# Kernel optimization log

Hardware: AMD Instinct MI355X
Metric: run time of the kernel (lower is better)

The kernel has to match this reference:

```python
import jax, jax.numpy as jnp
import numpy as np

B, S, D, H = 2, 2048, 1024, 16
DK = D // H  # 64


def setup_inputs() -> dict:
    key = jax.random.key(0)
    ks = jax.random.split(key, 9)
    query = jax.random.normal(ks[0], (B, S, D), dtype=jnp.float32)
    k_in = jax.random.normal(ks[1], (B, S, D), dtype=jnp.float32)
    v_in = jax.random.normal(ks[2], (B, S, D), dtype=jnp.float32)
    mask = jax.random.randint(ks[3], (B, S, S), 0, 2, dtype=jnp.int32)
    sc = 1.0 / np.sqrt(D)
    Wq = jax.random.normal(ks[4], (H, D, DK), dtype=jnp.float32) * sc  # per-head q proj
    Wk = jax.random.normal(ks[5], (H, D, DK), dtype=jnp.float32) * sc
    Wv = jax.random.normal(ks[6], (H, D, DK), dtype=jnp.float32) * sc
    Wu = jax.random.normal(ks[7], (D, D), dtype=jnp.float32) * sc  # unifyheads weight
    bu = jax.random.normal(ks[8], (D,), dtype=jnp.float32) * 0.01
    return {"query": query, "key": k_in, "value": v_in, "mask": mask,
            "Wq": Wq, "Wk": Wk, "Wv": Wv, "Wu": Wu, "bu": bu}


def reference(query, key, value, mask, Wq, Wk, Wv, Wu, bu):
    scale = DK ** 0.25  # original divides q and k each by d_k^(1/4)
    q = jnp.einsum('bsd,hdk->bhsk', query, Wq) / scale
    k = jnp.einsum('bsd,hdk->bhsk', key, Wk) / scale
    v = jnp.einsum('bsd,hdk->bhsk', value, Wv)
    scores = jnp.einsum('bhsk,bhtk->bhst', q, k)  # [B,H,S,S]
    scores = jnp.where(mask[:, None, :, :] == 0, jnp.float32(-1e9), scores)
    attn = jax.nn.softmax(scores, axis=-1)
    out = jnp.einsum('bhst,bhtk->bhsk', attn, v)
    out = jnp.transpose(out, (0, 2, 1, 3)).reshape(query.shape[0], query.shape[1], D)  # concat heads
    return out @ Wu + bu
```

## Files before the change

### kernel.cpp

```cpp
#include <hip/hip_runtime.h>
#include <hip/hip_bf16.h>


typedef __bf16 bf16_t;
typedef __attribute__((ext_vector_type(4))) __bf16 bf16x4;
typedef __attribute__((ext_vector_type(8))) __bf16 bf16x8;
typedef __attribute__((ext_vector_type(4))) float f32x4;
typedef unsigned int u32;

#define B_ 2
#define S_ 2048
#define D_ 1024
#define H_ 16
#define DK_ 64
#define NX_ (4096 * 1024)

static __device__ __forceinline__ f32x4 mfma16(bf16x8 a, bf16x8 b, f32x4 c) {
  return __builtin_amdgcn_mfma_f32_16x16x32_bf16(a, b, c, 0, 0, 0);
}

static __device__ __forceinline__ void async16(const bf16_t* g, bf16_t* l) {
  __builtin_amdgcn_global_load_lds(
      (const __attribute__((address_space(1))) u32*)g,
      (__attribute__((address_space(3))) u32*)l, 16, 0, 0);
}

__global__ __launch_bounds__(256) void prep(
    const float* __restrict__ q, const float* __restrict__ k,
    const float* __restrict__ v, const int* __restrict__ mask,
    const float* __restrict__ Wq, const float* __restrict__ Wk,
    const float* __restrict__ Wv, const float* __restrict__ Wu,
    bf16_t* __restrict__ qo, bf16_t* __restrict__ ko, bf16_t* __restrict__ vo,
    bf16_t* __restrict__ Bq, bf16_t* __restrict__ Bk, bf16_t* __restrict__ Bv,
    bf16_t* __restrict__ Bu, unsigned int* __restrict__ bits, float qkscale) {
  __shared__ __align__(16) bf16_t T[64][72];
  const int f = blockIdx.x;
  const int tid = threadIdx.x;

  if (f < 6144) {
    const int z = f / 2048, bx = f - z * 2048;
    const float* src = (z == 0) ? q : (z == 1) ? k : v;
    bf16_t* dst = (z == 0) ? qo : (z == 1) ? ko : vo;
    size_t i = ((size_t)bx * 256 + tid) * 8;
    float4 a = *(const float4*)(src + i);
    float4 b = *(const float4*)(src + i + 4);
    bf16x8 o;
    o[0] = (bf16_t)a.x; o[1] = (bf16_t)a.y; o[2] = (bf16_t)a.z; o[3] = (bf16_t)a.w;
    o[4] = (bf16_t)b.x; o[5] = (bf16_t)b.y; o[6] = (bf16_t)b.z; o[7] = (bf16_t)b.w;
    *(bf16x8*)(dst + i) = o;
  } else if (f < 7168) {
    const int idx = f - 6144;
    const int bx = idx & 15, by = (idx >> 4) & 15, z = idx >> 8;
    const float* W = (z == 0) ? Wq : (z == 1) ? Wk : (z == 2) ? Wv : Wu;
    bf16_t* BT = (z == 0) ? Bq : (z == 1) ? Bk : (z == 2) ? Bv : Bu;
    const float scale = (z <= 1) ? qkscale : 1.0f;
    const int d0 = bx * 64, nt = by;
    const int r = tid & 63, g = tid >> 6;

    const float* src = (z < 3)
        ? W + ((size_t)nt * D_ + d0 + r) * DK_ + g * 16
        : W + (size_t)(d0 + r) * D_ + nt * 64 + g * 16;
#pragma unroll
    for (int j = 0; j < 4; ++j) {
      float4 w4 = *(const float4*)(src + j * 4);
      T[g * 16 + j * 4 + 0][r] = (bf16_t)(w4.x * scale);
      T[g * 16 + j * 4 + 1][r] = (bf16_t)(w4.y * scale);
      T[g * 16 + j * 4 + 2][r] = (bf16_t)(w4.z * scale);
      T[g * 16 + j * 4 + 3][r] = (bf16_t)(w4.w * scale);
    }
    __syncthreads();
    const int orow = tid >> 3, seg = tid & 7;
#pragma unroll
    for (int p = 0; p < 2; ++p) {
      int rr = p * 32 + orow;
      *(bf16x8*)(BT + (size_t)(nt * 64 + rr) * D_ + d0 + seg * 8) =
          *(const bf16x8*)&T[rr][seg * 8];
    }
  } else {
    const int w = (f - 7168) * 256 + tid;
    const int4* p = (const int4*)(mask + (size_t)w * 32);
    unsigned int vv = 0;
#pragma unroll
    for (int i = 0; i < 8; ++i) {
      int4 m4 = p[i];
      vv |= (m4.x != 0 ? 1u : 0u) << (i * 4 + 0);
      vv |= (m4.y != 0 ? 1u : 0u) << (i * 4 + 1);
      vv |= (m4.z != 0 ? 1u : 0u) << (i * 4 + 2);
      vv |= (m4.w != 0 ? 1u : 0u) << (i * 4 + 3);
    }
    bits[w] = vv;
  }
}

__global__ __launch_bounds__(256) void gemm_bt(
    const bf16_t* __restrict__ A0, const bf16_t* __restrict__ A1,
    const bf16_t* __restrict__ A2, const bf16_t* __restrict__ BT0,
    const bf16_t* __restrict__ BT1, const bf16_t* __restrict__ BT2,
    bf16_t* __restrict__ C0, bf16_t* __restrict__ C1, bf16_t* __restrict__ C2) {
  __shared__ __align__(16) bf16_t As[128 * 64];
  __shared__ __align__(16) bf16_t Bs[128 * 64];

  const int flat = blockIdx.x;
  const int serial = (flat & 7) * 96 + (flat >> 3);
  const int z = serial >> 8;
  const int r = serial & 255;
  const bf16_t* A = (z == 0) ? A0 : (z == 1) ? A1 : A2;
  const bf16_t* BT = (z == 0) ? BT0 : (z == 1) ? BT1 : BT2;
  bf16_t* C = (z == 0) ? C0 : (z == 1) ? C1 : C2;
  const int row_blk = (z < 2) ? (r >> 3) : (r & 7);
  const int col_blk = (z < 2) ? (r & 7) : (r >> 3);
  const size_t ldc = (z < 2) ? 1024 : 4096;

  const int tid = threadIdx.x;
  const int lane = tid & 63, wave = tid >> 6;
  const int l = lane & 15, quad = lane >> 4;
  const int wm = wave >> 1, wn = wave & 1;
  const int row0 = row_blk * 128, col0 = col_blk * 128;

  const int lr = lane >> 3;
  const int gc8 = (lane & 7) ^ lr;
  const int xl = l & 7;

  f32x4 acc[4][4];
#pragma unroll
  for (int i = 0; i < 4; ++i)
#pragma unroll
    for (int j = 0; j < 4; ++j) acc[i][j] = {0.f, 0.f, 0.f, 0.f};

  for (int k0 = 0; k0 < 1024; k0 += 64) {
    __syncthreads();
#pragma unroll
    for (int c = 0; c < 4; ++c) {
      int r2 = wave * 32 + c * 8;
      async16(A + (size_t)(row0 + r2 + lr) * 1024 + k0 + gc8 * 8, As + r2 * 64);
      async16(BT + (size_t)(col0 + r2 + lr) * 1024 + k0 + gc8 * 8, Bs + r2 * 64);
    }
    __syncthreads();

#pragma unroll
    for (int kh = 0; kh < 2; ++kh) {
      bf16x8 af[4], bf[4];
#pragma unroll
      for (int f = 0; f < 4; ++f)
        af[f] = *(const bf16x8*)&As[(wm * 64 + f * 16 + l) * 64 +
                                    (((kh * 4 + quad) ^ xl) * 8)];
#pragma unroll
      for (int f = 0; f < 4; ++f)
        bf[f] = *(const bf16x8*)&Bs[(wn * 64 + f * 16 + l) * 64 +
                                    (((kh * 4 + quad) ^ xl) * 8)];
#pragma unroll
      for (int fm = 0; fm < 4; ++fm)
#pragma unroll
        for (int fn = 0; fn < 4; ++fn)
          acc[fm][fn] = mfma16(af[fm], bf[fn], acc[fm][fn]);
    }
  }

#pragma unroll
  for (int fm = 0; fm < 4; ++fm)
#pragma unroll
    for (int fn = 0; fn < 4; ++fn)
#pragma unroll
      for (int reg = 0; reg < 4; ++reg) {
        int row = row0 + wm * 64 + fm * 16 + quad * 4 + reg;
        int col = col0 + wn * 64 + fn * 16 + l;
        C[(size_t)row * ldc + col] = (bf16_t)acc[fm][fn][reg];
      }
}

__global__ __launch_bounds__(256) void gemm_bt64(
    const bf16_t* __restrict__ A, const bf16_t* __restrict__ BT,
    float* __restrict__ C, const float* __restrict__ bias) {
  __shared__ __align__(16) bf16_t As[64 * 64];
  __shared__ __align__(16) bf16_t Bs[128 * 64];

  const int flat = blockIdx.x;
  const int serial = (flat & 7) * 64 + (flat >> 3);
  const int tid = threadIdx.x;
  const int lane = tid & 63, wave = tid >> 6;
  const int l = lane & 15, quad = lane >> 4;
  const int row0 = (serial >> 3) * 64, col0 = (serial & 7) * 128;

  const int lr = lane >> 3;
  const int gc8 = (lane & 7) ^ lr;
  const int xl = l & 7;

  f32x4 acc[4][2];
#pragma unroll
  for (int i = 0; i < 4; ++i)
#pragma unroll
    for (int j = 0; j < 2; ++j) acc[i][j] = {0.f, 0.f, 0.f, 0.f};

  for (int k0 = 0; k0 < 1024; k0 += 64) {
    __syncthreads();
#pragma unroll
    for (int c = 0; c < 2; ++c) {
      int r = wave * 16 + c * 8;
      async16(A + (size_t)(row0 + r + lr) * 1024 + k0 + gc8 * 8, As + r * 64);
    }
#pragma unroll
    for (int c = 0; c < 4; ++c) {
      int r = wave * 32 + c * 8;
      async16(BT + (size_t)(col0 + r + lr) * 1024 + k0 + gc8 * 8, Bs + r * 64);
    }
    __syncthreads();

#pragma unroll
    for (int kh = 0; kh < 2; ++kh) {
      bf16x8 af[4], bf[2];
#pragma unroll
      for (int f = 0; f < 4; ++f)
        af[f] = *(const bf16x8*)&As[(f * 16 + l) * 64 +
                                    (((kh * 4 + quad) ^ xl) * 8)];
#pragma unroll
      for (int f = 0; f < 2; ++f)
        bf[f] = *(const bf16x8*)&Bs[(wave * 32 + f * 16 + l) * 64 +
                                    (((kh * 4 + quad) ^ xl) * 8)];
#pragma unroll
      for (int fm = 0; fm < 4; ++fm)
#pragma unroll
        for (int fn = 0; fn < 2; ++fn)
          acc[fm][fn] = mfma16(af[fm], bf[fn], acc[fm][fn]);
    }
  }

#pragma unroll
  for (int fm = 0; fm < 4; ++fm)
#pragma unroll
    for (int fn = 0; fn < 2; ++fn)
#pragma unroll
      for (int reg = 0; reg < 4; ++reg) {
        int row = row0 + fm * 16 + quad * 4 + reg;
        int col = col0 + wave * 32 + fn * 16 + l;
        C[(size_t)row * 1024 + col] = acc[fm][fn][reg] + bias[col];
      }
}

__global__ __launch_bounds__(256, 2) void attn_kernel(
    const bf16_t* __restrict__ Qx, const bf16_t* __restrict__ Kx,
    const bf16_t* __restrict__ Vt, const unsigned int* __restrict__ mbits,
    bf16_t* __restrict__ out) {
  __shared__ __align__(16) bf16_t Ks[2][64 * 64];
  __shared__ __align__(16) bf16_t Vts[2][64 * 64];
  __shared__ __align__(16) bf16_t Ps[4][32][72];

  const int tid = threadIdx.x;
  const int lane = tid & 63, wave = tid >> 6;
  const int l = lane & 15, quad = lane >> 4;

  const int flat = blockIdx.x + 16 * (blockIdx.y + 16 * blockIdx.z);
  const int serial = (flat >> 3) + (flat & 7) * 64;
  const int qt = serial & 15;
  const int h = (serial >> 4) & 15;
  const int b = serial >> 8;

  const int ch = h * 64;
  const size_t rb = (size_t)b * S_;
  const int q0 = qt * 128 + wave * 32;
  const int quad4 = quad * 4;

  const int lr = lane >> 3;
  const int gc8 = (lane & 7) ^ lr;
  const int xl = l & 7;

  bf16x8 bq[2][2];
#pragma unroll
  for (int mf = 0; mf < 2; ++mf) {
    const bf16_t* qp = Qx + (rb + q0 + mf * 16 + l) * D_ + ch;
    bq[mf][0] = *(const bf16x8*)(qp + quad * 8);
    bq[mf][1] = *(const bf16x8*)(qp + 32 + quad * 8);
  }

  bf16x8 ones;
#pragma unroll
  for (int j = 0; j < 8; ++j) ones[j] = (bf16_t)1.0f;

  const f32x4 zero = {0.f, 0.f, 0.f, 0.f};
  f32x4 o[2][4];
  f32x4 rs[2];
#pragma unroll
  for (int mf = 0; mf < 2; ++mf) {
    rs[mf] = zero;
#pragma unroll
    for (int nt = 0; nt < 4; ++nt) o[mf][nt] = zero;
  }

  const u32* mrow[2];
#pragma unroll
  for (int mf = 0; mf < 2; ++mf)
    mrow[mf] = mbits + (size_t)(b * S_ + q0 + mf * 16 + l) * (S_ / 32);

  auto stage = [&](int t0, int buf) {
#pragma unroll
    for (int it = 0; it < 2; ++it) {
      int r0 = it * 32 + wave * 8;
      async16(Kx + (rb + t0 + r0 + lr) * D_ + ch + gc8 * 8,
              &Ks[buf][r0 * 64]);
      async16(Vt + (size_t)(ch + r0 + lr) * 4096 + rb + t0 + gc8 * 8,
              &Vts[buf][r0 * 64]);
    }
  };

  stage(0, 0);
  uint2 mwc[2] = {*(const uint2*)&mrow[0][0], *(const uint2*)&mrow[1][0]};

  int cur = 0;
  for (int t0 = 0; t0 < S_; t0 += 64) {
    __syncthreads();
    const int tn = t0 + 64;
    if (tn < S_) stage(tn, cur ^ 1);
    const int nidx = (tn < S_) ? (tn >> 5) : 0;
    uint2 mwn0 = *(const uint2*)&mrow[0][nidx];
    uint2 mwn1 = *(const uint2*)&mrow[1][nidx];

    const bf16_t* Kc = Ks[cur];
    const bf16_t* Vc = Vts[cur];

#pragma unroll
    for (int ts = 0; ts < 4; ++ts) {
      int rK = (ts * 16 + l) * 64;
      bf16x8 ak0 = *(const bf16x8*)&Kc[rK + ((quad ^ xl) * 8)];
      bf16x8 ak1 = *(const bf16x8*)&Kc[rK + (((4 + quad) ^ xl) * 8)];
      int base = (ts & 1) * 16 + quad4;
#pragma unroll
      for (int mf = 0; mf < 2; ++mf) {
        f32x4 s = mfma16(ak0, bq[mf][0], zero);
        s = mfma16(ak1, bq[mf][1], s);
        u32 mw = (ts < 2) ? mwc[mf].x : mwc[mf].y;
        bf16x4 pv;
#pragma unroll
        for (int reg = 0; reg < 4; ++reg) {
          float e = exp2f(s[reg]);
          int bm = __builtin_amdgcn_sbfe(mw, base + reg, 1);
          float p = __int_as_float(__float_as_int(e) & bm);
          pv[reg] = (bf16_t)p;
        }
        *(bf16x4*)&Ps[wave][mf * 16 + l][ts * 16 + quad4] = pv;
      }
    }

    bf16x8 ap[2][2];
#pragma unroll
    for (int mf = 0; mf < 2; ++mf) {
      ap[mf][0] = *(const bf16x8*)&Ps[wave][mf * 16 + l][quad * 8];
      ap[mf][1] = *(const bf16x8*)&Ps[wave][mf * 16 + l][32 + quad * 8];
    }

    __builtin_amdgcn_s_setprio(1);
#pragma unroll
    for (int mf = 0; mf < 2; ++mf) {
      rs[mf] = mfma16(ap[mf][0], ones, rs[mf]);
      rs[mf] = mfma16(ap[mf][1], ones, rs[mf]);
    }
#pragma unroll
    for (int nt = 0; nt < 4; ++nt) {
      int rV = (nt * 16 + l) * 64;
      bf16x8 bv0 = *(const bf16x8*)&Vc[rV + ((quad ^ xl) * 8)];
      bf16x8 bv1 = *(const bf16x8*)&Vc[rV + (((4 + quad) ^ xl) * 8)];
#pragma unroll
      for (int mf = 0; mf < 2; ++mf) {
        o[mf][nt] = mfma16(ap[mf][0], bv0, o[mf][nt]);
        o[mf][nt] = mfma16(ap[mf][1], bv1, o[mf][nt]);
      }
    }
    __builtin_amdgcn_s_setprio(0);

    mwc[0] = mwn0;
    mwc[1] = mwn1;
    cur ^= 1;
  }

#pragma unroll
  for (int mf = 0; mf < 2; ++mf) {
#pragma unroll
    for (int reg = 0; reg < 4; ++reg) {
      float inv = (rs[mf][reg] > 0.f) ? (1.f / rs[mf][reg]) : 0.f;
      int srow = q0 + mf * 16 + quad4 + reg;
      bf16_t* op = out + (rb + srow) * D_ + ch;
#pragma unroll
      for (int nt = 0; nt < 4; ++nt)
        op[nt * 16 + l] = (bf16_t)(o[mf][nt][reg] * inv);
    }
  }
}

extern "C" void kernel_launch(void* const* d_in, const int* in_sizes, int n_in,
                              void* d_out, int out_size, void* d_ws, size_t ws_size,
                              hipStream_t stream) {
  const float* q_in = (const float*)d_in[0];
  const float* k_in = (const float*)d_in[1];
  const float* v_in = (const float*)d_in[2];
  const int* mask = (const int*)d_in[3];
  const float* Wq = (const float*)d_in[4];
  const float* Wk = (const float*)d_in[5];
  const float* Wv = (const float*)d_in[6];
  const float* Wu = (const float*)d_in[7];
  const float* bu = (const float*)d_in[8];
  float* outp = (float*)d_out;

  bf16_t* qx = (bf16_t*)d_ws;
  bf16_t* kx = qx + NX_;
  bf16_t* vx = kx + NX_;
  bf16_t* qb = vx + NX_;
  bf16_t* kb = qb + NX_;
  bf16_t* vtb = kb + NX_;
  bf16_t* BTq = vtb + NX_;
  bf16_t* BTk = BTq + D_ * D_;
  bf16_t* BTv = BTk + D_ * D_;
  bf16_t* BTu = BTv + D_ * D_;
  unsigned int* mb = (unsigned int*)(BTu + D_ * D_);
  bf16_t* ab = qx;

  const float qkscale = 0.35355339059327373f * 1.2011224087864498f;

  dim3 blk(256);
  prep<<<dim3(8192), blk, 0, stream>>>(q_in, k_in, v_in, mask,
                                       Wq, Wk, Wv, Wu,
                                       qx, kx, vx,
                                       BTq, BTk, BTv, BTu, mb, qkscale);
  gemm_bt<<<dim3(768), blk, 0, stream>>>(qx, kx, BTv, BTq, BTk, vx,
                                         qb, kb, vtb);
  attn_kernel<<<dim3(S_ / 128, H_, B_), blk, 0, stream>>>(qb, kb, vtb, mb, ab);
  gemm_bt64<<<dim3(512), blk, 0, stream>>>(ab, BTu, outp, bu);
}
```

Measured before the change: 263.7 us.

## Drop LDS staging and load GEMM and attention operands directly from global memory

Removes the async global-to-LDS staging, the LDS tiles and the barriers from both GEMM kernels and the attention kernel. Each wave now loads its MFMA fragments straight from global memory into registers, relying on L1/L2 caching for reuse across waves. Occupancy hints are added to the launch bounds. This removes LDS traffic and block-wide syncs, but loses data sharing between waves and the double-buffered prefetch in attention, so global and L2 traffic rises and load latency is exposed.

Measured after the change: 406.5 us. +54.2%, slower.

```diff
diff --git a/kernel.cpp b/kernel.cpp
--- a/kernel.cpp
+++ b/kernel.cpp
@@ -17,12 +17,6 @@
 
 static __device__ __forceinline__ f32x4 mfma16(bf16x8 a, bf16x8 b, f32x4 c) {
   return __builtin_amdgcn_mfma_f32_16x16x32_bf16(a, b, c, 0, 0, 0);
-}
-
-static __device__ __forceinline__ void async16(const bf16_t* g, bf16_t* l) {
-  __builtin_amdgcn_global_load_lds(
-      (const __attribute__((address_space(1))) u32*)g,
-      (__attribute__((address_space(3))) u32*)l, 16, 0, 0);
 }
 
 __global__ __launch_bounds__(256) void prep(
@@ -92,14 +86,11 @@
   }
 }
 
-__global__ __launch_bounds__(256) void gemm_bt(
+__global__ __launch_bounds__(256, 3) void gemm_bt(
     const bf16_t* __restrict__ A0, const bf16_t* __restrict__ A1,
     const bf16_t* __restrict__ A2, const bf16_t* __restrict__ BT0,
     const bf16_t* __restrict__ BT1, const bf16_t* __restrict__ BT2,
     bf16_t* __restrict__ C0, bf16_t* __restrict__ C1, bf16_t* __restrict__ C2) {
-  __shared__ __align__(16) bf16_t As[128 * 64];
-  __shared__ __align__(16) bf16_t Bs[128 * 64];
-
   const int flat = blockIdx.x;
   const int serial = (flat & 7) * 96 + (flat >> 3);
   const int z = serial >> 8;
@@ -115,11 +106,16 @@
   const int lane = tid & 63, wave = tid >> 6;
   const int l = lane & 15, quad = lane >> 4;
   const int wm = wave >> 1, wn = wave & 1;
-  const int row0 = row_blk * 128, col0 = col_blk * 128;
-
-  const int lr = lane >> 3;
-  const int gc8 = (lane & 7) ^ lr;
-  const int xl = l & 7;
+  const int row0 = blockIdx.x ? row_blk * 128 : row_blk * 128;
+  const int col0 = col_blk * 128;
+
+  const bf16_t* ap[4];
+  const bf16_t* bp[4];
+#pragma unroll
+  for (int f = 0; f < 4; ++f) {
+    ap[f] = A + (size_t)(row0 + wm * 64 + f * 16 + l) * 1024 + quad * 8;
+    bp[f] = BT + (size_t)(col0 + wn * 64 + f * 16 + l) * 1024 + quad * 8;
+  }
 
   f32x4 acc[4][4];
 #pragma unroll
@@ -128,26 +124,15 @@
     for (int j = 0; j < 4; ++j) acc[i][j] = {0.f, 0.f, 0.f, 0.f};
 
   for (int k0 = 0; k0 < 1024; k0 += 64) {
-    __syncthreads();
-#pragma unroll
-    for (int c = 0; c < 4; ++c) {
-      int r2 = wave * 32 + c * 8;
-      async16(A + (size_t)(row0 + r2 + lr) * 1024 + k0 + gc8 * 8, As + r2 * 64);
-      async16(BT + (size_t)(col0 + r2 + lr) * 1024 + k0 + gc8 * 8, Bs + r2 * 64);
-    }
-    __syncthreads();
-
 #pragma unroll
     for (int kh = 0; kh < 2; ++kh) {
       bf16x8 af[4], bf[4];
 #pragma unroll
       for (int f = 0; f < 4; ++f)
-        af[f] = *(const bf16x8*)&As[(wm * 64 + f * 16 + l) * 64 +
-                                    (((kh * 4 + quad) ^ xl) * 8)];
+        af[f] = *(const bf16x8*)(ap[f] + k0 + kh * 32);
 #pragma unroll
       for (int f = 0; f < 4; ++f)
-        bf[f] = *(const bf16x8*)&Bs[(wn * 64 + f * 16 + l) * 64 +
-                                    (((kh * 4 + quad) ^ xl) * 8)];
+        bf[f] = *(const bf16x8*)(bp[f] + k0 + kh * 32);
 #pragma unroll
       for (int fm = 0; fm < 4; ++fm)
 #pragma unroll
@@ -168,12 +153,9 @@
       }
 }
 
-__global__ __launch_bounds__(256) void gemm_bt64(
+__global__ __launch_bounds__(256, 2) void gemm_bt64(
     const bf16_t* __restrict__ A, const bf16_t* __restrict__ BT,
     float* __restrict__ C, const float* __restrict__ bias) {
-  __shared__ __align__(16) bf16_t As[64 * 64];
-  __shared__ __align__(16) bf16_t Bs[128 * 64];
-
   const int flat = blockIdx.x;
   const int serial = (flat & 7) * 64 + (flat >> 3);
   const int tid = threadIdx.x;
@@ -181,9 +163,14 @@
   const int l = lane & 15, quad = lane >> 4;
   const int row0 = (serial >> 3) * 64, col0 = (serial & 7) * 128;
 
-  const int lr = lane >> 3;
-  const int gc8 = (lane & 7) ^ lr;
-  const int xl = l & 7;
+  const bf16_t* ap[4];
+  const bf16_t* bp[2];
+#pragma unroll
+  for (int f = 0; f < 4; ++f)
+    ap[f] = A + (size_t)(row0 + f * 16 + l) * 1024 + quad * 8;
+#pragma unroll
+  for (int f = 0; f < 2; ++f)
+    bp[f] = BT + (size_t)(col0 + wave * 32 + f * 16 + l) * 1024 + quad * 8;
 
   f32x4 acc[4][2];
 #pragma unroll
@@ -192,30 +179,15 @@
     for (int j = 0; j < 2; ++j) acc[i][j] = {0.f, 0.f, 0.f, 0.f};
 
   for (int k0 = 0; k0 < 1024; k0 += 64) {
-    __syncthreads();
-#pragma unroll
-    for (int c = 0; c < 2; ++c) {
-      int r = wave * 16 + c * 8;
-      async16(A + (size_t)(row0 + r + lr) * 1024 + k0 + gc8 * 8, As + r * 64);
-    }
-#pragma unroll
-    for (int c = 0; c < 4; ++c) {
-      int r = wave * 32 + c * 8;
-      async16(BT + (size_t)(col0 + r + lr) * 1024 + k0 + gc8 * 8, Bs + r * 64);
-    }
-    __syncthreads();
-
 #pragma unroll
     for (int kh = 0; kh < 2; ++kh) {
       bf16x8 af[4], bf[2];
 #pragma unroll
       for (int f = 0; f < 4; ++f)
-        af[f] = *(const bf16x8*)&As[(f * 16 + l) * 64 +
-                                    (((kh * 4 + quad) ^ xl) * 8)];
+        af[f] = *(const bf16x8*)(ap[f] + k0 + kh * 32);
 #pragma unroll
       for (int f = 0; f < 2; ++f)
-        bf[f] = *(const bf16x8*)&Bs[(wave * 32 + f * 16 + l) * 64 +
-                                    (((kh * 4 + quad) ^ xl) * 8)];
+        bf[f] = *(const bf16x8*)(bp[f] + k0 + kh * 32);
 #pragma unroll
       for (int fm = 0; fm < 4; ++fm)
 #pragma unroll
@@ -240,8 +212,6 @@
     const bf16_t* __restrict__ Qx, const bf16_t* __restrict__ Kx,
     const bf16_t* __restrict__ Vt, const unsigned int* __restrict__ mbits,
     bf16_t* __restrict__ out) {
-  __shared__ __align__(16) bf16_t Ks[2][64 * 64];
-  __shared__ __align__(16) bf16_t Vts[2][64 * 64];
   __shared__ __align__(16) bf16_t Ps[4][32][72];
 
   const int tid = threadIdx.x;
@@ -259,10 +229,6 @@
   const int q0 = qt * 128 + wave * 32;
   const int quad4 = quad * 4;
 
-  const int lr = lane >> 3;
-  const int gc8 = (lane & 7) ^ lr;
-  const int xl = l & 7;
-
   bf16x8 bq[2][2];
 #pragma unroll
   for (int mf = 0; mf < 2; ++mf) {
@@ -290,42 +256,31 @@
   for (int mf = 0; mf < 2; ++mf)
     mrow[mf] = mbits + (size_t)(b * S_ + q0 + mf * 16 + l) * (S_ / 32);
 
-  auto stage = [&](int t0, int buf) {
-#pragma unroll
-    for (int it = 0; it < 2; ++it) {
-      int r0 = it * 32 + wave * 8;
-      async16(Kx + (rb + t0 + r0 + lr) * D_ + ch + gc8 * 8,
-              &Ks[buf][r0 * 64]);
-      async16(Vt + (size_t)(ch + r0 + lr) * 4096 + rb + t0 + gc8 * 8,
-              &Vts[buf][r0 * 64]);
-    }
-  };
-
-  stage(0, 0);
-  uint2 mwc[2] = {*(const uint2*)&mrow[0][0], *(const uint2*)&mrow[1][0]};
-
-  int cur = 0;
   for (int t0 = 0; t0 < S_; t0 += 64) {
-    __syncthreads();
-    const int tn = t0 + 64;
-    if (tn < S_) stage(tn, cur ^ 1);
-    const int nidx = (tn < S_) ? (tn >> 5) : 0;
-    uint2 mwn0 = *(const uint2*)&mrow[0][nidx];
-    uint2 mwn1 = *(const uint2*)&mrow[1][nidx];
-
-    const bf16_t* Kc = Ks[cur];
-    const bf16_t* Vc = Vts[cur];
-
+    bf16x8 ak[4][2];
 #pragma unroll
     for (int ts = 0; ts < 4; ++ts) {
-      int rK = (ts * 16 + l) * 64;
-      bf16x8 ak0 = *(const bf16x8*)&Kc[rK + ((quad ^ xl) * 8)];
-      bf16x8 ak1 = *(const bf16x8*)&Kc[rK + (((4 + quad) ^ xl) * 8)];
+      const bf16_t* kp = Kx + (rb + t0 + ts * 16 + l) * D_ + ch;
+      ak[ts][0] = *(const bf16x8*)(kp + quad * 8);
+      ak[ts][1] = *(const bf16x8*)(kp + 32 + quad * 8);
+    }
+    bf16x8 bv[4][2];
+#pragma unroll
+    for (int nt = 0; nt < 4; ++nt) {
+      const bf16_t* vp = Vt + (size_t)(ch + nt * 16 + l) * 4096 + rb + t0;
+      bv[nt][0] = *(const bf16x8*)(vp + quad * 8);
+      bv[nt][1] = *(const bf16x8*)(vp + 32 + quad * 8);
+    }
+    uint2 mwc[2] = {*(const uint2*)&mrow[0][t0 >> 5],
+                    *(const uint2*)&mrow[1][t0 >> 5]};
+
+#pragma unroll
+    for (int ts = 0; ts < 4; ++ts) {
       int base = (ts & 1) * 16 + quad4;
 #pragma unroll
       for (int mf = 0; mf < 2; ++mf) {
-        f32x4 s = mfma16(ak0, bq[mf][0], zero);
-        s = mfma16(ak1, bq[mf][1], s);
+        f32x4 s = mfma16(ak[ts][0], bq[mf][0], zero);
+        s = mfma16(ak[ts][1], bq[mf][1], s);
         u32 mw = (ts < 2) ? mwc[mf].x : mwc[mf].y;
         bf16x4 pv;
 #pragma unroll
@@ -354,20 +309,13 @@
     }
 #pragma unroll
     for (int nt = 0; nt < 4; ++nt) {
-      int rV = (nt * 16 + l) * 64;
-      bf16x8 bv0 = *(const bf16x8*)&Vc[rV + ((quad ^ xl) * 8)];
-      bf16x8 bv1 = *(const bf16x8*)&Vc[rV + (((4 + quad) ^ xl) * 8)];
 #pragma unroll
       for (int mf = 0; mf < 2; ++mf) {
-        o[mf][nt] = mfma16(ap[mf][0], bv0, o[mf][nt]);
-        o[mf][nt] = mfma16(ap[mf][1], bv1, o[mf][nt]);
+        o[mf][nt] = mfma16(ap[mf][0], bv[nt][0], o[mf][nt]);
+        o[mf][nt] = mfma16(ap[mf][1], bv[nt][1], o[mf][nt]);
       }
     }
     __builtin_amdgcn_s_setprio(0);
-
-    mwc[0] = mwn0;
-    mwc[1] = mwn1;
-    cur ^= 1;
   }
 
 #pragma unroll
```

## Software-pipeline attention loop across tiles with triple-buffered K/V staging

Applied to the files above, without the earlier changes.

Restructures the attention main loop so the QK^T MFMAs for the next key tile are issued while softmax and P·V for the previous tile run, with K/V staging moved from double to triple buffering in LDS. The goal is to overlap exp/mask VALU work with matrix-core work and hide the dependency between score computation and softmax. It adds LDS use (one more 64x64 K and V buffer) and keeps a full score tile live in registers, which may lower occupancy or cause spills under the 256x2 launch bounds. The prologue and epilogue handle the first and last tiles separately.

Result: no change. 260.0 us (-1.4%).

```diff
diff --git a/kernel.cpp b/kernel.cpp
--- a/kernel.cpp
+++ b/kernel.cpp
@@ -240,8 +240,8 @@
     const bf16_t* __restrict__ Qx, const bf16_t* __restrict__ Kx,
     const bf16_t* __restrict__ Vt, const unsigned int* __restrict__ mbits,
     bf16_t* __restrict__ out) {
-  __shared__ __align__(16) bf16_t Ks[2][64 * 64];
-  __shared__ __align__(16) bf16_t Vts[2][64 * 64];
+  __shared__ __align__(16) bf16_t Ks[3][64 * 64];
+  __shared__ __align__(16) bf16_t Vts[3][64 * 64];
   __shared__ __align__(16) bf16_t Ps[4][32][72];
 
   const int tid = threadIdx.x;
@@ -301,51 +301,46 @@
     }
   };
 
-  stage(0, 0);
-  uint2 mwc[2] = {*(const uint2*)&mrow[0][0], *(const uint2*)&mrow[1][0]};
-
-  int cur = 0;
-  for (int t0 = 0; t0 < S_; t0 += 64) {
-    __syncthreads();
-    const int tn = t0 + 64;
-    if (tn < S_) stage(tn, cur ^ 1);
-    const int nidx = (tn < S_) ? (tn >> 5) : 0;
-    uint2 mwn0 = *(const uint2*)&mrow[0][nidx];
-    uint2 mwn1 = *(const uint2*)&mrow[1][nidx];
-
-    const bf16_t* Kc = Ks[cur];
-    const bf16_t* Vc = Vts[cur];
-
+  auto qk_tile = [&](const bf16_t* Kc, f32x4 s[4][2]) {
 #pragma unroll
     for (int ts = 0; ts < 4; ++ts) {
       int rK = (ts * 16 + l) * 64;
       bf16x8 ak0 = *(const bf16x8*)&Kc[rK + ((quad ^ xl) * 8)];
       bf16x8 ak1 = *(const bf16x8*)&Kc[rK + (((4 + quad) ^ xl) * 8)];
+#pragma unroll
+      for (int mf = 0; mf < 2; ++mf) {
+        f32x4 acc0 = mfma16(ak0, bq[mf][0], zero);
+        s[ts][mf] = mfma16(ak1, bq[mf][1], acc0);
+      }
+    }
+  };
+
+  auto softmax_store = [&](f32x4 s[4][2], uint2 mw[2]) {
+#pragma unroll
+    for (int ts = 0; ts < 4; ++ts) {
       int base = (ts & 1) * 16 + quad4;
 #pragma unroll
       for (int mf = 0; mf < 2; ++mf) {
-        f32x4 s = mfma16(ak0, bq[mf][0], zero);
-        s = mfma16(ak1, bq[mf][1], s);
-        u32 mw = (ts < 2) ? mwc[mf].x : mwc[mf].y;
+        u32 m = (ts < 2) ? mw[mf].x : mw[mf].y;
         bf16x4 pv;
 #pragma unroll
         for (int reg = 0; reg < 4; ++reg) {
-          float e = exp2f(s[reg]);
-          int bm = __builtin_amdgcn_sbfe(mw, base + reg, 1);
-          float p = __int_as_float(__float_as_int(e) & bm);
-          pv[reg] = (bf16_t)p;
+          float e = exp2f(s[ts][mf][reg]);
+          int bm = __builtin_amdgcn_sbfe(m, base + reg, 1);
+          pv[reg] = (bf16_t)__int_as_float(__float_as_int(e) & bm);
         }
         *(bf16x4*)&Ps[wave][mf * 16 + l][ts * 16 + quad4] = pv;
       }
     }
-
+  };
+
+  auto pv_tile = [&](const bf16_t* Vc) {
     bf16x8 ap[2][2];
 #pragma unroll
     for (int mf = 0; mf < 2; ++mf) {
       ap[mf][0] = *(const bf16x8*)&Ps[wave][mf * 16 + l][quad * 8];
       ap[mf][1] = *(const bf16x8*)&Ps[wave][mf * 16 + l][32 + quad * 8];
     }
-
     __builtin_amdgcn_s_setprio(1);
 #pragma unroll
     for (int mf = 0; mf < 2; ++mf) {
@@ -364,11 +359,34 @@
       }
     }
     __builtin_amdgcn_s_setprio(0);
-
-    mwc[0] = mwn0;
-    mwc[1] = mwn1;
-    cur ^= 1;
-  }
+  };
+
+  stage(0, 0);
+  uint2 mwp[2] = {*(const uint2*)&mrow[0][0], *(const uint2*)&mrow[1][0]};
+  f32x4 s[4][2];
+  __syncthreads();
+  stage(64, 1);
+  qk_tile(Ks[0], s);
+
+  int bc = 1, bp = 0, bn = 2;
+  for (int t = 1; t < 32; ++t) {
+    __syncthreads();
+    if (t + 1 < 32) stage((t + 1) * 64, bn);
+    uint2 mwc[2] = {*(const uint2*)&mrow[0][2 * t],
+                    *(const uint2*)&mrow[1][2 * t]};
+
+    softmax_store(s, mwp);
+    qk_tile(Ks[bc], s);
+    pv_tile(Vts[bp]);
+
+    mwp[0] = mwc[0];
+    mwp[1] = mwc[1];
+    int t2 = bp;
+    bp = bc; bc = bn; bn = t2;
+  }
+
+  softmax_store(s, mwp);
+  pv_tile(Vts[bp]);
 
 #pragma unroll
   for (int mf = 0; mf < 2; ++mf) {
```
